# Performance work log

Hardware: AMD Instinct MI355X
Metric: run time of the kernel (lower is better)

Reference implementation:

```python
import jax, jax.numpy as jnp
import numpy as np
from jax.ops import segment_sum

N = 100000
E = 1600000
D_IN = 64
D_H = 64
D_OUT = 16


def _gcn_norm(edge_index, n_nodes):
    # PyG GCNConv default: add self-loops, symmetric normalization.
    src, dst = edge_index[0], edge_index[1]
    loop = jnp.arange(n_nodes, dtype=edge_index.dtype)
    src = jnp.concatenate([src, loop])
    dst = jnp.concatenate([dst, loop])
    deg = segment_sum(jnp.ones(src.shape[0], dtype=jnp.float32), dst, num_segments=n_nodes)
    dinv = jnp.where(deg > 0, jax.lax.rsqrt(deg), 0.0)
    norm = dinv[src] * dinv[dst]  # [E + N]
    return src, dst, norm


def _gcn_layer(x, W, b, src, dst, norm, n_nodes):
    h = x @ W  # dense transform first (out_channels <= in_channels)
    msg = h[src] * norm[:, None]          # gather + scale  [E+N, out]
    agg = segment_sum(msg, dst, num_segments=n_nodes)  # scatter-add
    return agg + b


def setup_inputs() -> dict:
    key = jax.random.key(0)
    ks = jax.random.split(key, 10)
    x = jax.random.normal(ks[0], (N, D_IN), dtype=jnp.float32)
    edge_index = jax.random.randint(ks[1], (2, E), 0, N, dtype=jnp.int64)

    def glorot(k, fan_in, fan_out):
        lim = np.sqrt(6.0 / (fan_in + fan_out)).astype(np.float32)
        return jax.random.uniform(k, (fan_in, fan_out), jnp.float32, -lim, lim)

    return {
        "x": x,
        "edge_index": edge_index,
        "W1": glorot(ks[2], D_IN, D_H), "b1": jnp.zeros((D_H,), jnp.float32),
        "W2": glorot(ks[3], D_H, D_H), "b2": jnp.zeros((D_H,), jnp.float32),
        "W3": glorot(ks[4], D_H, D_H), "b3": jnp.zeros((D_H,), jnp.float32),
        "W4": glorot(ks[5], D_H, D_OUT), "b4": jnp.zeros((D_OUT,), jnp.float32),
    }


def reference(x, edge_index, W1, b1, W2, b2, W3, b3, W4, b4):
    n = x.shape[0]
    src, dst, norm = _gcn_norm(edge_index, n)
    h = jax.nn.relu(_gcn_layer(x, W1, b1, src, dst, norm, n))
    h = jax.nn.relu(_gcn_layer(h, W2, b2, src, dst, norm, n))
    h = jax.nn.relu(_gcn_layer(h, W3, b3, src, dst, norm, n))
    return _gcn_layer(h, W4, b4, src, dst, norm, n)
```

## Files before the change

kernel.cpp:

```cpp
#include <hip/hip_runtime.h>
#include <hip/hip_fp16.h>

#define NN 100000
#define NE 1600000
#define BK 512
#define BKSH 9
#define NBKT 196
#define SLOT 9216
#define SRCMASK 0x1FFFF

typedef _Float16 half2v __attribute__((ext_vector_type(2)));

__device__ inline float dot2acc(unsigned int a, unsigned int b, float c) {
#if __has_builtin(__builtin_amdgcn_fdot2)
    union { unsigned int u; half2v h; } ua, ub;
    ua.u = a; ub.u = b;
    return __builtin_amdgcn_fdot2(ua.h, ub.h, c, false);
#else
    float2 fa = __half22float2(*(const __half2*)&a);
    float2 fb = __half22float2(*(const __half2*)&b);
    return c + fa.x * fb.x + fa.y * fb.y;
#endif
}

__device__ inline int wave_incl_scan(int v, int lane) {
#pragma unroll
    for (int off = 1; off < 64; off <<= 1) {
        int t = __shfl_up(v, off, 64);
        if (lane >= off) v += t;
    }
    return v;
}


__global__ __launch_bounds__(256) void zero_small_kernel(int* __restrict__ p, int n) {
    int i = threadIdx.x + blockIdx.x * 256;
    if (i < n) p[i] = 0;
}

__global__ __launch_bounds__(512) void bscatter_kernel(const int* __restrict__ src,
                                                       const int* __restrict__ dst,
                                                       int* __restrict__ bcur,
                                                       unsigned int* __restrict__ bedges,
                                                       int e) {
    __shared__ int h[256];
    __shared__ int sc[256];
    __shared__ int gb[256];
    __shared__ int2 stg[4096];
    int tid = threadIdx.x;
    int tile = blockIdx.x * 4096;
    int cnt_tile = min(4096, e - tile);
    if (tid < 256) h[tid] = 0;
    __syncthreads();
    unsigned int pk[8]; int rk[8], bk[8];
#pragma unroll
    for (int j = 0; j < 8; j++) {
        int li = tid + j * 512;
        if (li < cnt_tile) {
            int s = src[tile + li];
            int d = dst[tile + li];
            bk[j] = d >> BKSH;
            pk[j] = ((unsigned)(d & (BK - 1)) << 17) | (unsigned)s;
            rk[j] = atomicAdd(&h[bk[j]], 1);
        } else bk[j] = -1;
    }
    __syncthreads();
    if (tid < 64) {
        int b0 = tid * 4;
        int c0 = h[b0], c1 = h[b0 + 1], c2 = h[b0 + 2], c3 = h[b0 + 3];
        int s4 = c0 + c1 + c2 + c3;
        int incl = wave_incl_scan(s4, tid);
        int base = incl - s4;
        sc[b0] = base; sc[b0 + 1] = base + c0;
        sc[b0 + 2] = base + c0 + c1; sc[b0 + 3] = base + c0 + c1 + c2;
        if (c0) gb[b0] = atomicAdd(&bcur[b0], c0);
        if (c1) gb[b0 + 1] = atomicAdd(&bcur[b0 + 1], c1);
        if (c2) gb[b0 + 2] = atomicAdd(&bcur[b0 + 2], c2);
        if (c3) gb[b0 + 3] = atomicAdd(&bcur[b0 + 3], c3);
    }
    __syncthreads();
#pragma unroll
    for (int j = 0; j < 8; j++)
        if (bk[j] >= 0) stg[sc[bk[j]] + rk[j]] = make_int2((int)pk[j], bk[j]);
    __syncthreads();
#pragma unroll
    for (int j = 0; j < 8; j++) {
        int li = tid + j * 512;
        if (li < cnt_tile) {
            int2 p2 = stg[li];
            int b = p2.y;
            bedges[(size_t)b * SLOT + gb[b] + (li - sc[b])] = (unsigned int)p2.x;
        }
    }
}

__global__ __launch_bounds__(1024) void bfill_kernel(const unsigned int* __restrict__ bedges,
                                                     const int* __restrict__ bcur,
                                                     const float* __restrict__ x,
                                                     int* __restrict__ start,
                                                     int* __restrict__ cnt,
                                                     float* __restrict__ dinv,
                                                     int* __restrict__ csr,
                                                     __half* __restrict__ g) {
    __shared__ int lcnt[BK];
    __shared__ int lstart[BK];
    __shared__ int lcur[BK];
    __shared__ unsigned int sbuf[SLOT];
    int q = blockIdx.x, tid = threadIdx.x;
    size_t ebase = (size_t)q * SLOT;
    int ec = bcur[q];
    int nbase = q * BK;
    if (tid < BK) lcnt[tid] = 0;
    __syncthreads();
    unsigned int pk[9];
#pragma unroll
    for (int k = 0; k < 9; k++) {
        int i = tid + k * 1024;
        pk[k] = (i < ec) ? __builtin_nontemporal_load(&bedges[ebase + i]) : 0xFFFFFFFFu;
    }
#pragma unroll
    for (int k = 0; k < 9; k++)
        if (pk[k] != 0xFFFFFFFFu) atomicAdd(&lcnt[pk[k] >> 17], 1);
    __syncthreads();
    if (tid < 64) {
        int b0 = tid * 8;
        int c[8]; int s = 0;
#pragma unroll
        for (int k = 0; k < 8; k++) { c[k] = lcnt[b0 + k]; s += c[k]; }
        int incl = wave_incl_scan(s, tid);
        int run = incl - s;
#pragma unroll
        for (int k = 0; k < 8; k++) { lstart[b0 + k] = run; lcur[b0 + k] = run; run += c[k]; }
    }
    __syncthreads();
    if (tid < BK) {
        int nd = nbase + tid;
        if (nd < NN) {
            start[nd] = (int)ebase + lstart[tid];
            cnt[nd]   = lcnt[tid];
            dinv[nd]  = rsqrtf((float)lcnt[tid] + 1.0f);
        }
    }
#pragma unroll
    for (int k = 0; k < 9; k++) {
        if (pk[k] != 0xFFFFFFFFu) {
            int r = atomicAdd(&lcur[pk[k] >> 17], 1);
            sbuf[r] = pk[k] & SRCMASK;
        }
    }
    __syncthreads();
    for (int i = tid; i < ec; i += 1024)
        csr[ebase + i] = (int)sbuf[i];
    int nh = NN - nbase; if (nh > BK) nh = BK;
    for (int i = tid; i < nh * 16; i += 1024) {
        int r = i >> 4, c4 = (i & 15) << 2;
        float dvv = rsqrtf((float)lcnt[r] + 1.0f);
        size_t off = (size_t)(nbase + r) * 64 + c4;
        float4 v = *(const float4*)&x[off];
        union { __half2 h[2]; uint2 u; } pq;
        pq.h[0] = __floats2half2_rn(v.x * dvv, v.y * dvv);
        pq.h[1] = __floats2half2_rn(v.z * dvv, v.w * dvv);
        *(uint2*)&g[off] = pq.u;
    }
}

__global__ __launch_bounds__(512) void fused_layer_kernel(const __half* __restrict__ g,
                                                          const int* __restrict__ csr,
                                                          const int* __restrict__ start,
                                                          const int* __restrict__ cnt,
                                                          const float* __restrict__ dinv,
                                                          const float* __restrict__ Wg,
                                                          const float* __restrict__ bias,
                                                          __half* __restrict__ gout, int n) {
    __shared__ uint4 wpk[8][64];
    __shared__ __half zh[8][64];
    __shared__ float bs[64];
    int tid = threadIdx.x;
    {
        int p = tid >> 6, c = tid & 63;
        float w[8];
#pragma unroll
        for (int i = 0; i < 8; i++) w[i] = Wg[(8 * p + i) * 64 + c];
        union { __half2 h; unsigned int u; } u0, u1, u2, u3;
        u0.h = __floats2half2_rn(w[0], w[1]);
        u1.h = __floats2half2_rn(w[2], w[3]);
        u2.h = __floats2half2_rn(w[4], w[5]);
        u3.h = __floats2half2_rn(w[6], w[7]);
        wpk[p][c] = make_uint4(u0.u, u1.u, u2.u, u3.u);
    }
    if (tid < 64) bs[tid] = bias[tid];
    __syncthreads();

    int wv = tid >> 6, lane = tid & 63;
    int node = blockIdx.x * 8 + wv;
    float acc = 0.f;
    float dv = 0.f;
    if (node < n) {
        int st = __builtin_amdgcn_readfirstlane(start[node]);
        int cn = __builtin_amdgcn_readfirstlane(cnt[node]);
        dv = dinv[node];
        acc = __half2float(g[(size_t)node * 64 + lane]);
        int iv = 0;
        if (cn > 0) iv = __builtin_nontemporal_load(&csr[st + (lane < cn ? lane : cn - 1)]);
        int cs = cn > 64 ? 64 : cn;
        int e = 0;
        for (; e + 7 < cs; e += 8) {
            int u[8]; float a[8];
#pragma unroll
            for (int j = 0; j < 8; j++) u[j] = __shfl(iv, e + j, 64);
#pragma unroll
            for (int j = 0; j < 8; j++) a[j] = __half2float(g[(size_t)u[j] * 64 + lane]);
            acc += ((a[0] + a[1]) + (a[2] + a[3])) + ((a[4] + a[5]) + (a[6] + a[7]));
        }
        for (; e + 3 < cs; e += 4) {
            int u0 = __shfl(iv, e + 0, 64);
            int u1 = __shfl(iv, e + 1, 64);
            int u2 = __shfl(iv, e + 2, 64);
            int u3 = __shfl(iv, e + 3, 64);
            float a0 = __half2float(g[(size_t)u0 * 64 + lane]);
            float a1 = __half2float(g[(size_t)u1 * 64 + lane]);
            float a2 = __half2float(g[(size_t)u2 * 64 + lane]);
            float a3 = __half2float(g[(size_t)u3 * 64 + lane]);
            acc += (a0 + a1) + (a2 + a3);
        }
        for (; e < cs; e++) {
            int u = __shfl(iv, e, 64);
            acc += __half2float(g[(size_t)u * 64 + lane]);
        }
        for (; e < cn; e++) {
            int u = __builtin_nontemporal_load(&csr[st + e]);
            acc += __half2float(g[(size_t)u * 64 + lane]);
        }
    }
    zh[wv][lane] = __float2half_rn(acc);
    if (node < n) {
        float t = 0.f;
#pragma unroll
        for (int p = 0; p < 8; p++) {
            uint4 wq = wpk[p][lane];
            uint4 zq = *(const uint4*)&zh[wv][p * 8];
            t = dot2acc(zq.x, wq.x, t);
            t = dot2acc(zq.y, wq.y, t);
            t = dot2acc(zq.z, wq.z, t);
            t = dot2acc(zq.w, wq.w, t);
        }
        float o = dv * t + bs[lane];
        o = fmaxf(o, 0.f);
        gout[(size_t)node * 64 + lane] = __float2half_rn(dv * o);
    }
}

__global__ __launch_bounds__(128) void gemm16_kernel(const __half* __restrict__ xin,
                                                     const float* __restrict__ W,
                                                     __half* __restrict__ s, int n) {
    constexpr int DOUT = 16;
    constexpr int ROWS = 128;
    __shared__ float xs[ROWS][65];
    __shared__ float ws[64][DOUT];
    int tid = threadIdx.x;
    int row0 = blockIdx.x * ROWS;
    for (int i = tid; i < 64 * DOUT; i += 128) ws[i / DOUT][i % DOUT] = W[i];
    for (int i = tid; i < ROWS * 16; i += 128) {
        int r = i >> 4, c = (i & 15) * 4;
        float4 v = make_float4(0.f, 0.f, 0.f, 0.f);
        if (row0 + r < n) {
            const __half* hp = xin + (size_t)(row0 + r) * 64 + c;
            float2 f01 = __half22float2(*(const __half2*)hp);
            float2 f23 = __half22float2(*(const __half2*)(hp + 2));
            v = make_float4(f01.x, f01.y, f23.x, f23.y);
        }
        xs[r][c] = v.x; xs[r][c + 1] = v.y; xs[r][c + 2] = v.z; xs[r][c + 3] = v.w;
    }
    __syncthreads();
    int rbase = tid;
    float acc[16];
#pragma unroll
    for (int j = 0; j < 16; j++) acc[j] = 0.f;
    for (int k = 0; k < 64; k++) {
        float xv = xs[rbase][k];
#pragma unroll
        for (int j = 0; j < 4; j++) {
            float4 wv = *(const float4*)&ws[k][j * 4];
            acc[j * 4 + 0] += xv * wv.x;
            acc[j * 4 + 1] += xv * wv.y;
            acc[j * 4 + 2] += xv * wv.z;
            acc[j * 4 + 3] += xv * wv.w;
        }
    }
    int r = row0 + rbase;
    if (r < n) {
        union { ushort u[16]; uint4 q[2]; } pk;
#pragma unroll
        for (int j = 0; j < 16; j++)
            pk.u[j] = __half_as_ushort(__float2half_rn(acc[j]));
        uint4* sp = (uint4*)&s[(size_t)r * DOUT];
        sp[0] = pk.q[0];
        sp[1] = pk.q[1];
    }
}

__global__ __launch_bounds__(256) void agg16_kernel(const __half* __restrict__ s,
                                                    const int* __restrict__ csr,
                                                    const int* __restrict__ start,
                                                    const int* __restrict__ cnt,
                                                    const float* __restrict__ dinv,
                                                    const float* __restrict__ bias,
                                                    float* __restrict__ out, int n) {
    constexpr int D = 16;
    int tid = threadIdx.x;
    int lane = tid & 63;
    int wave = tid >> 6;
    int col = lane % D;
    int grp = lane / D;
    int node = (blockIdx.x * 4 + wave) * 4 + grp;
    if (node >= n) return;
    int st = start[node];
    int cn = cnt[node];
    float acc = __half2float(s[(size_t)node * D + col]);
    int e = 0;
    for (; e + 7 < cn; e += 8) {
        int u[8]; float a[8];
#pragma unroll
        for (int j = 0; j < 8; j++) u[j] = __builtin_nontemporal_load(&csr[st + e + j]);
#pragma unroll
        for (int j = 0; j < 8; j++) a[j] = __half2float(s[(size_t)u[j] * D + col]);
        acc += ((a[0] + a[1]) + (a[2] + a[3])) + ((a[4] + a[5]) + (a[6] + a[7]));
    }
    for (; e + 3 < cn; e += 4) {
        int u0 = __builtin_nontemporal_load(&csr[st + e + 0]);
        int u1 = __builtin_nontemporal_load(&csr[st + e + 1]);
        int u2 = __builtin_nontemporal_load(&csr[st + e + 2]);
        int u3 = __builtin_nontemporal_load(&csr[st + e + 3]);
        float a0 = __half2float(s[(size_t)u0 * D + col]);
        float a1 = __half2float(s[(size_t)u1 * D + col]);
        float a2 = __half2float(s[(size_t)u2 * D + col]);
        float a3 = __half2float(s[(size_t)u3 * D + col]);
        acc += (a0 + a1) + (a2 + a3);
    }
    for (; e < cn; e++) {
        int u = __builtin_nontemporal_load(&csr[st + e]);
        acc += __half2float(s[(size_t)u * D + col]);
    }
    float o = dinv[node] * acc + bias[col];
    __builtin_nontemporal_store(o, out + (size_t)node * D + col);
}


extern "C" void kernel_launch(void* const* d_in, const int* in_sizes, int n_in,
                              void* d_out, int out_size, void* d_ws, size_t ws_size,
                              hipStream_t stream) {
    const float* x  = (const float*)d_in[0];
    const int* ei   = (const int*)d_in[1];
    const float* W1 = (const float*)d_in[2];
    const float* b1 = (const float*)d_in[3];
    const float* W2 = (const float*)d_in[4];
    const float* b2 = (const float*)d_in[5];
    const float* W3 = (const float*)d_in[6];
    const float* b3 = (const float*)d_in[7];
    const float* W4 = (const float*)d_in[8];
    const float* b4 = (const float*)d_in[9];
    const int* src = ei;
    const int* dst = ei + NE;

    char* w = (char*)d_ws;
    float* dinv  = (float*)w;          w += (size_t)NN * 4;
    int* cnt     = (int*)w;            w += (size_t)NN * 4;
    int* start   = (int*)w;            w += (size_t)NN * 4;
    int* bcur    = (int*)w;            w += (size_t)256 * 4;
    int* csr     = (int*)w;            w += (size_t)NBKT * SLOT * 4;
    __half* gA   = (__half*)w;         w += (size_t)NN * 64 * 2;
    __half* gB   = (__half*)w;         w += (size_t)NN * 64 * 2;
    __half* s4   = (__half*)w;         w += (size_t)NN * 16 * 2;
    unsigned int* bedges = (unsigned int*)w;  w += (size_t)NBKT * SLOT * 4;

    zero_small_kernel<<<1, 256, 0, stream>>>(bcur, 256);
    bscatter_kernel<<<(NE + 4095) / 4096, 512, 0, stream>>>(src, dst, bcur, bedges, NE);
    bfill_kernel<<<NBKT, 1024, 0, stream>>>(bedges, bcur, x, start, cnt, dinv, csr, gA);

    const int FB = (NN + 7) / 8;
    fused_layer_kernel<<<FB, 512, 0, stream>>>(gA, csr, start, cnt, dinv, W1, b1, gB, NN);
    fused_layer_kernel<<<FB, 512, 0, stream>>>(gB, csr, start, cnt, dinv, W2, b2, gA, NN);
    fused_layer_kernel<<<FB, 512, 0, stream>>>(gA, csr, start, cnt, dinv, W3, b3, gB, NN);

    const int GB = (NN + 127) / 128;
    const int AB16 = (NN + 15) / 16;
    gemm16_kernel<<<GB, 128, 0, stream>>>(gB, W4, s4, NN);
    agg16_kernel<<<AB16, 256, 0, stream>>>(s4, csr, start, cnt, dinv, b4, (float*)d_out, NN);
}
```

Measured before the change: 351.1 us.

## Fuse final 64x16 projection into third layer kernel, simplify neighbor index loading

The third fused GCN layer now also applies the W4 projection in-kernel with packed fp16 dot products and writes the 16-wide result directly. This removes the separate gemm16 kernel and the round trip of the 64-wide layer-3 output through memory. Neighbor indices are now read straight from the CSR array inside the gather loops instead of one coalesced preload followed by wave shuffles. The zero kernel is also replaced by hipMemsetAsync. The index-load change may add scalar or vector load latency per edge in exchange for fewer shuffles.

```diff
diff --git a/kernel.cpp b/kernel.cpp
--- a/kernel.cpp
+++ b/kernel.cpp
@@ -32,11 +32,6 @@
     return v;
 }
 
-
-__global__ __launch_bounds__(256) void zero_small_kernel(int* __restrict__ p, int n) {
-    int i = threadIdx.x + blockIdx.x * 256;
-    if (i < n) p[i] = 0;
-}
 
 __global__ __launch_bounds__(512) void bscatter_kernel(const int* __restrict__ src,
                                                        const int* __restrict__ dst,
@@ -164,6 +159,7 @@
     }
 }
 
+template<int LAST>
 __global__ __launch_bounds__(512) void fused_layer_kernel(const __half* __restrict__ g,
                                                           const int* __restrict__ csr,
                                                           const int* __restrict__ start,
@@ -171,9 +167,13 @@
                                                           const float* __restrict__ dinv,
                                                           const float* __restrict__ Wg,
                                                           const float* __restrict__ bias,
-                                                          __half* __restrict__ gout, int n) {
+                                                          const float* __restrict__ W4,
+                                                          __half* __restrict__ gout,
+                                                          __half* __restrict__ s4out, int n) {
     __shared__ uint4 wpk[8][64];
     __shared__ __half zh[8][64];
+    __shared__ __half z2[8][64];
+    __shared__ uint4 w4pk[8][16];
     __shared__ float bs[64];
     int tid = threadIdx.x;
     {
@@ -187,6 +187,18 @@
         u2.h = __floats2half2_rn(w[4], w[5]);
         u3.h = __floats2half2_rn(w[6], w[7]);
         wpk[p][c] = make_uint4(u0.u, u1.u, u2.u, u3.u);
+    }
+    if (LAST && tid < 128) {
+        int p = tid >> 4, j = tid & 15;
+        float w[8];
+#pragma unroll
+        for (int i = 0; i < 8; i++) w[i] = W4[(8 * p + i) * 16 + j];
+        union { __half2 h; unsigned int u; } u0, u1, u2, u3;
+        u0.h = __floats2half2_rn(w[0], w[1]);
+        u1.h = __floats2half2_rn(w[2], w[3]);
+        u2.h = __floats2half2_rn(w[4], w[5]);
+        u3.h = __floats2half2_rn(w[6], w[7]);
+        w4pk[p][j] = make_uint4(u0.u, u1.u, u2.u, u3.u);
     }
     if (tid < 64) bs[tid] = bias[tid];
     __syncthreads();
@@ -200,32 +212,25 @@
         int cn = __builtin_amdgcn_readfirstlane(cnt[node]);
         dv = dinv[node];
         acc = __half2float(g[(size_t)node * 64 + lane]);
-        int iv = 0;
-        if (cn > 0) iv = __builtin_nontemporal_load(&csr[st + (lane < cn ? lane : cn - 1)]);
-        int cs = cn > 64 ? 64 : cn;
         int e = 0;
-        for (; e + 7 < cs; e += 8) {
+        for (; e + 7 < cn; e += 8) {
             int u[8]; float a[8];
 #pragma unroll
-            for (int j = 0; j < 8; j++) u[j] = __shfl(iv, e + j, 64);
+            for (int j = 0; j < 8; j++) u[j] = __builtin_nontemporal_load(&csr[st + e + j]);
 #pragma unroll
             for (int j = 0; j < 8; j++) a[j] = __half2float(g[(size_t)u[j] * 64 + lane]);
             acc += ((a[0] + a[1]) + (a[2] + a[3])) + ((a[4] + a[5]) + (a[6] + a[7]));
         }
-        for (; e + 3 < cs; e += 4) {
-            int u0 = __shfl(iv, e + 0, 64);
-            int u1 = __shfl(iv, e + 1, 64);
-            int u2 = __shfl(iv, e + 2, 64);
-            int u3 = __shfl(iv, e + 3, 64);
+        for (; e + 3 < cn; e += 4) {
+            int u0 = __builtin_nontemporal_load(&csr[st + e + 0]);
+            int u1 = __builtin_nontemporal_load(&csr[st + e + 1]);
+            int u2 = __builtin_nontemporal_load(&csr[st + e + 2]);
+            int u3 = __builtin_nontemporal_load(&csr[st + e + 3]);
             float a0 = __half2float(g[(size_t)u0 * 64 + lane]);
             float a1 = __half2float(g[(size_t)u1 * 64 + lane]);
             float a2 = __half2float(g[(size_t)u2 * 64 + lane]);
             float a3 = __half2float(g[(size_t)u3 * 64 + lane]);
             acc += (a0 + a1) + (a2 + a3);
-        }
-        for (; e < cs; e++) {
-            int u = __shfl(iv, e, 64);
-            acc += __half2float(g[(size_t)u * 64 + lane]);
         }
         for (; e < cn; e++) {
             int u = __builtin_nontemporal_load(&csr[st + e]);
@@ -246,56 +251,25 @@
         }
         float o = dv * t + bs[lane];
         o = fmaxf(o, 0.f);
-        gout[(size_t)node * 64 + lane] = __float2half_rn(dv * o);
-    }
-}
-
-__global__ __launch_bounds__(128) void gemm16_kernel(const __half* __restrict__ xin,
-                                                     const float* __restrict__ W,
-                                                     __half* __restrict__ s, int n) {
-    constexpr int DOUT = 16;
-    constexpr int ROWS = 128;
-    __shared__ float xs[ROWS][65];
-    __shared__ float ws[64][DOUT];
-    int tid = threadIdx.x;
-    int row0 = blockIdx.x * ROWS;
-    for (int i = tid; i < 64 * DOUT; i += 128) ws[i / DOUT][i % DOUT] = W[i];
-    for (int i = tid; i < ROWS * 16; i += 128) {
-        int r = i >> 4, c = (i & 15) * 4;
-        float4 v = make_float4(0.f, 0.f, 0.f, 0.f);
-        if (row0 + r < n) {
-            const __half* hp = xin + (size_t)(row0 + r) * 64 + c;
-            float2 f01 = __half22float2(*(const __half2*)hp);
-            float2 f23 = __half22float2(*(const __half2*)(hp + 2));
-            v = make_float4(f01.x, f01.y, f23.x, f23.y);
-        }
-        xs[r][c] = v.x; xs[r][c + 1] = v.y; xs[r][c + 2] = v.z; xs[r][c + 3] = v.w;
-    }
-    __syncthreads();
-    int rbase = tid;
-    float acc[16];
-#pragma unroll
-    for (int j = 0; j < 16; j++) acc[j] = 0.f;
-    for (int k = 0; k < 64; k++) {
-        float xv = xs[rbase][k];
-#pragma unroll
-        for (int j = 0; j < 4; j++) {
-            float4 wv = *(const float4*)&ws[k][j * 4];
-            acc[j * 4 + 0] += xv * wv.x;
-            acc[j * 4 + 1] += xv * wv.y;
-            acc[j * 4 + 2] += xv * wv.z;
-            acc[j * 4 + 3] += xv * wv.w;
-        }
-    }
-    int r = row0 + rbase;
-    if (r < n) {
-        union { ushort u[16]; uint4 q[2]; } pk;
-#pragma unroll
-        for (int j = 0; j < 16; j++)
-            pk.u[j] = __half_as_ushort(__float2half_rn(acc[j]));
-        uint4* sp = (uint4*)&s[(size_t)r * DOUT];
-        sp[0] = pk.q[0];
-        sp[1] = pk.q[1];
+        float g3 = dv * o;
+        if (!LAST) {
+            gout[(size_t)node * 64 + lane] = __float2half_rn(g3);
+        } else {
+            z2[wv][lane] = __float2half_rn(g3);
+            if (lane < 16) {
+                float t4 = 0.f;
+#pragma unroll
+                for (int p = 0; p < 8; p++) {
+                    uint4 wq = w4pk[p][lane];
+                    uint4 zq = *(const uint4*)&z2[wv][p * 8];
+                    t4 = dot2acc(zq.x, wq.x, t4);
+                    t4 = dot2acc(zq.y, wq.y, t4);
+                    t4 = dot2acc(zq.z, wq.z, t4);
+                    t4 = dot2acc(zq.w, wq.w, t4);
+                }
+                s4out[(size_t)node * 16 + lane] = __float2half_rn(t4);
+            }
+        }
     }
 }
 
@@ -373,17 +347,15 @@
     __half* s4   = (__half*)w;         w += (size_t)NN * 16 * 2;
     unsigned int* bedges = (unsigned int*)w;  w += (size_t)NBKT * SLOT * 4;
 
-    zero_small_kernel<<<1, 256, 0, stream>>>(bcur, 256);
+    hipMemsetAsync(bcur, 0, 256 * sizeof(int), stream);
     bscatter_kernel<<<(NE + 4095) / 4096, 512, 0, stream>>>(src, dst, bcur, bedges, NE);
     bfill_kernel<<<NBKT, 1024, 0, stream>>>(bedges, bcur, x, start, cnt, dinv, csr, gA);
 
     const int FB = (NN + 7) / 8;
-    fused_layer_kernel<<<FB, 512, 0, stream>>>(gA, csr, start, cnt, dinv, W1, b1, gB, NN);
-    fused_layer_kernel<<<FB, 512, 0, stream>>>(gB, csr, start, cnt, dinv, W2, b2, gA, NN);
-    fused_layer_kernel<<<FB, 512, 0, stream>>>(gA, csr, start, cnt, dinv, W3, b3, gB, NN);
-
-    const int GB = (NN + 127) / 128;
+    fused_layer_kernel<0><<<FB, 512, 0, stream>>>(gA, csr, start, cnt, dinv, W1, b1, W4, gB, s4, NN);
+    fused_layer_kernel<0><<<FB, 512, 0, stream>>>(gB, csr, start, cnt, dinv, W2, b2, W4, gA, s4, NN);
+    fused_layer_kernel<1><<<FB, 512, 0, stream>>>(gA, csr, start, cnt, dinv, W3, b3, W4, gB, s4, NN);
+
     const int AB16 = (NN + 15) / 16;
-    gemm16_kernel<<<GB, 128, 0, stream>>>(gB, W4, s4, NN);
     agg16_kernel<<<AB16, 256, 0, stream>>>(s4, csr, start, cnt, dinv, b4, (float*)d_out, NN);
 }
```

Measured after the change: 324.4 us. -7.6%, faster.
